# Kernel tuning notes

Hardware: AMD Instinct MI355X
Metric: run time of the kernel (lower is better)

The kernel has to match this reference:

```python
import jax, jax.numpy as jnp
import numpy as np

LAT = 512
FIN = 256
FOUT = 256
K = 3
N_STYLE = 4
B, H, W = 16, 64, 64


def setup_inputs() -> dict:
    key = jax.random.key(0)
    ks = jax.random.split(key, 8)
    x = jax.random.normal(ks[0], (B, FIN, H, W), dtype=jnp.float32)
    lat = jax.random.normal(ks[1], (B, LAT), dtype=jnp.float32)
    # main conv weight, kaiming_normal fan_in, leaky_relu a=0 -> gain sqrt(2)
    fan_in = FIN * K * K
    weight = jax.random.normal(ks[2], (FOUT, FIN, K, K), dtype=jnp.float32) * np.float32(np.sqrt(2.0 / fan_in))
    # EqualLinear layers: raw weight ~ N(0,1), runtime-scaled by 1/sqrt(in_dim)
    ws = jax.random.normal(ks[3], (N_STYLE, LAT, LAT), dtype=jnp.float32)
    bs = jnp.zeros((N_STYLE, LAT), dtype=jnp.float32)
    # final plain nn.Linear(lat_size, fin): uniform(-1/sqrt(in), 1/sqrt(in))
    bound = np.float32(1.0 / np.sqrt(LAT))
    wf = jax.random.uniform(ks[4], (FIN, LAT), dtype=jnp.float32, minval=-bound, maxval=bound)
    bf = jax.random.uniform(ks[5], (FIN,), dtype=jnp.float32, minval=-bound, maxval=bound)
    return {"x": x, "lat": lat, "weight": weight, "ws": ws, "bs": bs, "wf": wf, "bf": bf}


def reference(x, lat, weight, ws, bs, wf, bf):
    Bb, fin, Hh, Ww = x.shape
    fout, _, k, _ = weight.shape
    eq_scale = np.float32(1.0 / np.sqrt(lat.shape[1]))  # EqualLinear runtime scale

    # style MLP: n_layers_style x (EqualLinear + LeakyReLU(0.2)), then Linear -> fin
    h = lat
    for i in range(ws.shape[0]):
        h = jax.nn.leaky_relu(h @ (ws[i] * eq_scale).T + bs[i], 0.2)
    styles = h @ wf.T + bf  # [B, fin]

    # normalize base weight by inf-norm over (fin,k,k) per output channel
    wnorm = jnp.max(jnp.abs(weight), axis=(1, 2, 3), keepdims=True)
    mw = weight * (np.float32(1.0 / np.sqrt(fin * k * k)) / wnorm)  # [fout,fin,k,k]
    # normalize styles by inf-norm per sample
    styles = styles / jnp.max(jnp.abs(styles), axis=1, keepdims=True)

    # per-sample modulation + demodulation
    w = mw[None] * styles[:, None, :, None, None]  # [B,fout,fin,k,k]
    dcoefs = jax.lax.rsqrt(jnp.sum(w * w, axis=(2, 3, 4)) + 1e-8)  # [B,fout]
    w = w * dcoefs[:, :, None, None, None]
    w = w.reshape(Bb * fout, fin, k, k)

    # grouped conv with groups = batch (stride/dilation NOT passed in original -> 1)
    pad = (k - 1) // 2  # _get_same_padding with stride=1, dilation=1
    xg = x.reshape(1, Bb * fin, Hh, Ww)
    y = jax.lax.conv_general_dilated(
        xg, w, window_strides=(1, 1), padding=[(pad, pad), (pad, pad)],
        dimension_numbers=("NCHW", "OIHW", "NCHW"), feature_group_count=Bb)
    return y.reshape(Bb, fout, Hh, Ww)
```

## Files before the change

### kernel.cpp

```cpp
#include <hip/hip_runtime.h>
#include <hip/hip_bf16.h>

#define LATN 512
#define FINN 256
#define FOUTN 256
#define NB 16
#define HH 64
#define WW 64

typedef __attribute__((ext_vector_type(8))) short bf16x8;
typedef __attribute__((ext_vector_type(4))) float f32x4;
typedef __attribute__((ext_vector_type(4))) int i32x4;

#define WS_MW2    4096
#define WS_DCO    266240
#define WS_STY    282624
#define WS_WFMT   299008
#define WS_XM     1478656
#define WS_HA     (WS_XM)
#define WS_HB     (WS_XM + 32768)

__global__ void weight_prep_kernel(const float* __restrict__ weight,
                                   __hip_bfloat16* __restrict__ wfmt,
                                   float* __restrict__ mw2sum) {
    __shared__ float red[256];
    int o = blockIdx.x, t = threadIdx.x;
    const float* wrow = weight + ((size_t)o * FINN + t) * 9;
    float wv[9];
    float mx = 0.f;
    #pragma unroll
    for (int k = 0; k < 9; ++k) { wv[k] = wrow[k]; mx = fmaxf(mx, fabsf(wv[k])); }
    red[t] = mx;
    __syncthreads();
    for (int k = 128; k > 0; k >>= 1) {
        if (t < k) red[t] = fmaxf(red[t], red[t + k]);
        __syncthreads();
    }
    float scale = (1.0f / 48.0f) / red[0];
    int obi = o >> 6, ol = o & 63, ch = t >> 5, il = t & 31;
    int slot = (il >> 3) ^ ((ol >> 1) & 3);
    char* basep = (char*)wfmt + (size_t)obi * 294912 + (size_t)ch * 36864
                + (size_t)ol * 64 + slot * 16 + (il & 7) * 2;
    float s2 = 0.f;
    #pragma unroll
    for (int tap = 0; tap < 9; ++tap) {
        float m = wv[tap] * scale;
        s2 += m * m;
        *(__hip_bfloat16*)(basep + tap * 4096) = __float2bfloat16(m);
    }
    mw2sum[(size_t)o * FINN + t] = s2;
}

__global__ __launch_bounds__(256) void style_layer_kernel(
    const float* __restrict__ in, const float* __restrict__ w,
    const float* __restrict__ bias, float* __restrict__ out,
    int in_dim_v4, int out_dim, float scale, int do_lrelu) {
    int t = threadIdx.x;
    int jl = t >> 4, kl = t & 15;
    int j = blockIdx.x * 16 + jl;
    int b = blockIdx.y;
    const float4* inr = (const float4*)(in + (size_t)b * (in_dim_v4 * 4));
    const float4* wr  = (const float4*)(w + (size_t)j * (in_dim_v4 * 4));
    float sum = 0.f;
    #pragma unroll 4
    for (int kb = kl; kb < in_dim_v4; kb += 16) {
        float4 wv = wr[kb], iv = inr[kb];
        sum += wv.x * iv.x + wv.y * iv.y + wv.z * iv.z + wv.w * iv.w;
    }
    #pragma unroll
    for (int off = 8; off >= 1; off >>= 1)
        sum += __shfl_xor(sum, off, 16);
    if (kl == 0) {
        float v = sum * scale + bias[j];
        if (do_lrelu && v < 0.f) v *= 0.2f;
        out[(size_t)b * out_dim + j] = v;
    }
}

__global__ __launch_bounds__(256) void xcvt_kernel(const float* __restrict__ x,
                                                   const float* __restrict__ sty,
                                                   const float* __restrict__ mw2,
                                                   float* __restrict__ dco,
                                                   char* __restrict__ xm) {
    __shared__ float tile[64][65];
    __shared__ float styl[256];
    int h = blockIdx.x, b = blockIdx.y;
    int t = threadIdx.x;
    int lane = t & 63;
    int wl_ = t & 63, ig = t >> 6;
    const float* styb = sty + (size_t)b * FINN;
    float mxv = 0.f;
    #pragma unroll
    for (int q = 0; q < 4; ++q) mxv = fmaxf(mxv, fabsf(styb[lane + 64 * q]));
    #pragma unroll
    for (int off = 32; off >= 1; off >>= 1) mxv = fmaxf(mxv, __shfl_xor(mxv, off));
    float inv_m = 1.0f / mxv;
    styl[t] = styb[t] * inv_m;
    __syncthreads();

    if (h < 4) {
        int o_l = t >> 2, kl = t & 3;
        int o = h * 64 + o_l;
        const float4* m2r = (const float4*)(mw2 + (size_t)o * FINN) + kl * 16;
        const float4* svr = (const float4*)styl + kl * 16;
        float sum = 0.f;
        #pragma unroll
        for (int kb = 0; kb < 16; ++kb) {
            float4 a = m2r[kb], v = svr[kb];
            sum += a.x * v.x * v.x + a.y * v.y * v.y + a.z * v.z * v.z + a.w * v.w * v.w;
        }
        sum += __shfl_xor(sum, 1);
        sum += __shfl_xor(sum, 2);
        if (kl == 0) dco[(size_t)b * FOUTN + o] = rsqrtf(sum + 1e-8f);
    }

    char* xmb = xm + (size_t)b * 2097152;
    for (int icb = 0; icb < 4; ++icb) {
        if (icb) __syncthreads();
        #pragma unroll
        for (int p = 0; p < 16; ++p) {
            int i_l = p * 4 + ig;
            int i = icb * 64 + i_l;
            tile[i_l][wl_] = x[((size_t)(b * FINN + i)) * 4096 + h * 64 + wl_] * styl[i];
        }
        __syncthreads();
        #pragma unroll
        for (int rep = 0; rep < 2; ++rep) {
            int g = rep * 256 + t;
            int w = g >> 3, q8 = g & 7;
            int chunk = icb * 2 + (q8 >> 2), iq = q8 & 3;
            int slot = iq ^ (((h + 1) + ((w + 1) >> 1)) & 3);
            short tmp[8];
            #pragma unroll
            for (int j = 0; j < 8; ++j) {
                __hip_bfloat16 hb = __float2bfloat16(tile[q8 * 8 + j][w]);
                tmp[j] = *(short*)&hb;
            }
            char* dst = xmb + (size_t)chunk * 262144 + (size_t)(h * 64 + w) * 64 + slot * 16;
            *(bf16x8*)dst = *(bf16x8*)tmp;
        }
    }
}

__device__ __forceinline__ void gl_lds16(const void* g, void* l) {
    __builtin_amdgcn_global_load_lds(
        (const __attribute__((address_space(1))) unsigned int*)g,
        (__attribute__((address_space(3))) unsigned int*)l, 16, 0, 0);
}

template<int KH, int KW>
__device__ __forceinline__ void do_tap(f32x4 acc[4][8], bf16x8 rb[3][4],
                                       const char* xs, const char* wl,
                                       int wid, int l15, int lg, int wfrag) {
    constexpr int tap = KH * 3 + KW;
    bf16x8 wf[4], ra[4], nb[4];
    #pragma unroll
    for (int mt = 0; mt < 4; ++mt)
        wf[mt] = *(const bf16x8*)(wl + tap * 4096 + mt * 1024 + wfrag);
    if (KH == 0) {
        int p0 = (wid * 2) * 66 + KW + l15;
        int ba = p0 * 64 + ((lg ^ ((p0 >> 1) & 3)) << 4);
        #pragma unroll
        for (int nt = 0; nt < 4; ++nt)
            ra[nt] = *(const bf16x8*)(xs + ba + nt * 1024);
    }
    {
        int p1 = (wid * 2 + KH + 1) * 66 + KW + l15;
        int bb = p1 * 64 + ((lg ^ ((p1 >> 1) & 3)) << 4);
        #pragma unroll
        for (int nt = 0; nt < 4; ++nt)
            nb[nt] = *(const bf16x8*)(xs + bb + nt * 1024);
    }
    __builtin_amdgcn_sched_barrier(0);
    asm volatile("s_waitcnt lgkmcnt(4)" ::: "memory");
    __builtin_amdgcn_sched_barrier(0);
    __builtin_amdgcn_s_setprio(1);
    #pragma unroll
    for (int mt = 0; mt < 4; ++mt)
        #pragma unroll
        for (int nt = 0; nt < 4; ++nt)
            acc[mt][nt] = __builtin_amdgcn_mfma_f32_16x16x32_bf16(
                wf[mt], (KH == 0) ? ra[nt] : rb[KW][nt], acc[mt][nt], 0, 0, 0);
    __builtin_amdgcn_s_setprio(0);
    __builtin_amdgcn_sched_barrier(0);
    asm volatile("s_waitcnt lgkmcnt(0)" ::: "memory");
    __builtin_amdgcn_sched_barrier(0);
    __builtin_amdgcn_s_setprio(1);
    #pragma unroll
    for (int mt = 0; mt < 4; ++mt)
        #pragma unroll
        for (int nt = 0; nt < 4; ++nt)
            acc[mt][4 + nt] = __builtin_amdgcn_mfma_f32_16x16x32_bf16(
                wf[mt], nb[nt], acc[mt][4 + nt], 0, 0, 0);
    __builtin_amdgcn_s_setprio(0);
    #pragma unroll
    for (int nt = 0; nt < 4; ++nt) rb[KW][nt] = nb[nt];
}

__global__ __launch_bounds__(256, 2) void mconv_kernel(
    const char* __restrict__ xm, const char* __restrict__ wfmt,
    const float* __restrict__ dco, float* __restrict__ y) {
    __shared__ char xs[42240];
    __shared__ char wl[36864];

    int t = threadIdx.x;
    int lane = t & 63;
    int wid = t >> 6;
    int h0 = blockIdx.x * 8;
    int obi = blockIdx.y;
    int b = blockIdx.z;

    if (t < 80) {
        int r = t >> 3, sub = t & 7;
        int col = (sub >> 2) * 65, slot = sub & 3;
        *(i32x4*)(xs + ((r * 66 + col) * 4 + slot) * 16) = (i32x4){0, 0, 0, 0};
    }
    if (h0 == 0) {
        int e = t;
        *(i32x4*)(xs + ((0 * 66 + 1 + (e >> 2)) * 4 + (e & 3)) * 16) = (i32x4){0, 0, 0, 0};
    }
    if (h0 == 56) {
        int e = t;
        *(i32x4*)(xs + ((9 * 66 + 1 + (e >> 2)) * 4 + (e & 3)) * 16) = (i32x4){0, 0, 0, 0};
    }

    const char* xmb = xm + (size_t)b * 2097152 + lane * 16;
    unsigned xoff[10], xdst[10];
    #pragma unroll
    for (int q = 0; q < 10; ++q) {
        int idx = wid * 10 + q;
        int r = idx >> 2, quarter = idx & 3;
        int gh = h0 - 1 + r;
        bool v = (gh >= 0) && (gh < HH);
        xoff[q] = (unsigned)__builtin_amdgcn_readfirstlane(
            v ? (int)((gh * 64 + quarter * 16) * 64) : (int)0xFFFFFFFF);
        xdst[q] = (unsigned)__builtin_amdgcn_readfirstlane(
            (int)((r * 66 + 1) * 64 + quarter * 1024));
    }
    const char* wlane = wfmt + (size_t)obi * 294912 + lane * 16;

    f32x4 acc[4][8] = {};
    int l15 = lane & 15, lg = lane >> 4;
    int wfrag = l15 * 64 + ((lg ^ ((l15 >> 1) & 3)) << 4);

    for (int ch = 0; ch < 8; ++ch) {
        const char* xch = xmb + (size_t)ch * 262144;
        #pragma unroll
        for (int q = 0; q < 10; ++q)
            if (xoff[q] != 0xFFFFFFFFu) gl_lds16(xch + xoff[q], xs + xdst[q]);
        const char* wch = wlane + (size_t)ch * 36864;
        #pragma unroll
        for (int q = 0; q < 9; ++q)
            gl_lds16(wch + (wid + q * 4) * 1024, wl + (wid + q * 4) * 1024);
        asm volatile("s_waitcnt vmcnt(0) lgkmcnt(0)" ::: "memory");
        __builtin_amdgcn_s_barrier();
        __builtin_amdgcn_sched_barrier(0);

        {
            bf16x8 rb[3][4];
            do_tap<0, 0>(acc, rb, xs, wl, wid, l15, lg, wfrag);
            do_tap<0, 1>(acc, rb, xs, wl, wid, l15, lg, wfrag);
            do_tap<0, 2>(acc, rb, xs, wl, wid, l15, lg, wfrag);
            do_tap<1, 0>(acc, rb, xs, wl, wid, l15, lg, wfrag);
            do_tap<1, 1>(acc, rb, xs, wl, wid, l15, lg, wfrag);
            do_tap<1, 2>(acc, rb, xs, wl, wid, l15, lg, wfrag);
            do_tap<2, 0>(acc, rb, xs, wl, wid, l15, lg, wfrag);
            do_tap<2, 1>(acc, rb, xs, wl, wid, l15, lg, wfrag);
            do_tap<2, 2>(acc, rb, xs, wl, wid, l15, lg, wfrag);
        }

        __builtin_amdgcn_s_barrier();
        __builtin_amdgcn_sched_barrier(0);
    }

    const float* dcb = dco + (size_t)b * FOUTN + obi * 64;
    #pragma unroll
    for (int rr = 0; rr < 2; ++rr) {
        float* yb = y + (((size_t)b * FOUTN + obi * 64) * HH + (h0 + wid * 2 + rr)) * WW;
        #pragma unroll
        for (int mt = 0; mt < 4; ++mt) {
            #pragma unroll
            for (int j = 0; j < 4; ++j) {
                int o_l = mt * 16 + lg * 4 + j;
                float d = dcb[o_l];
                #pragma unroll
                for (int n4 = 0; n4 < 4; ++n4)
                    yb[(size_t)o_l * 4096 + n4 * 16 + l15] = acc[mt][rr * 4 + n4][j] * d;
            }
        }
    }
}

extern "C" void kernel_launch(void* const* d_in, const int* in_sizes, int n_in,
                              void* d_out, int out_size, void* d_ws, size_t ws_size,
                              hipStream_t stream) {
    const float* x      = (const float*)d_in[0];
    const float* lat    = (const float*)d_in[1];
    const float* weight = (const float*)d_in[2];
    const float* wsm    = (const float*)d_in[3];
    const float* bsm    = (const float*)d_in[4];
    const float* wff    = (const float*)d_in[5];
    const float* bff    = (const float*)d_in[6];
    float* y = (float*)d_out;

    char* base = (char*)d_ws;
    float* mw2     = (float*)(base + WS_MW2);
    float* dco     = (float*)(base + WS_DCO);
    float* sty     = (float*)(base + WS_STY);
    __hip_bfloat16* wfmt = (__hip_bfloat16*)(base + WS_WFMT);
    char* xm       = base + WS_XM;
    float* hA      = (float*)(base + WS_HA);
    float* hB      = (float*)(base + WS_HB);

    const float eq = 0.044194173824159216f;

    weight_prep_kernel<<<FOUTN, 256, 0, stream>>>(weight, wfmt, mw2);
    style_layer_kernel<<<dim3(LATN / 16, NB), 256, 0, stream>>>(
        lat, wsm + 0 * (size_t)LATN * LATN, bsm + 0 * LATN, hA, LATN / 4, LATN, eq, 1);
    style_layer_kernel<<<dim3(LATN / 16, NB), 256, 0, stream>>>(
        hA, wsm + 1 * (size_t)LATN * LATN, bsm + 1 * LATN, hB, LATN / 4, LATN, eq, 1);
    style_layer_kernel<<<dim3(LATN / 16, NB), 256, 0, stream>>>(
        hB, wsm + 2 * (size_t)LATN * LATN, bsm + 2 * LATN, hA, LATN / 4, LATN, eq, 1);
    style_layer_kernel<<<dim3(LATN / 16, NB), 256, 0, stream>>>(
        hA, wsm + 3 * (size_t)LATN * LATN, bsm + 3 * LATN, hB, LATN / 4, LATN, eq, 1);
    style_layer_kernel<<<dim3(FINN / 16, NB), 256, 0, stream>>>(
        hB, wff, bff, sty, LATN / 4, FINN, 1.0f, 0);
    xcvt_kernel<<<dim3(HH, NB), 256, 0, stream>>>(x, sty, mw2, dco, xm);
    mconv_kernel<<<dim3(8, 4, NB), 256, 0, stream>>>(xm, (const char*)wfmt, dco, y);
}
```

Before: 109.8 us.

## Fuse style scaling and bf16 conversion of x into conv kernel tile loads

New measurement: 108.7 us. About the same (-1.1%).

```diff
diff --git a/kernel.cpp b/kernel.cpp
--- a/kernel.cpp
+++ b/kernel.cpp
@@ -19,6 +19,7 @@
 #define WS_XM     1478656
 #define WS_HA     (WS_XM)
 #define WS_HB     (WS_XM + 32768)
+#define WS_SNORM  (WS_XM + 65536)
 
 __global__ void weight_prep_kernel(const float* __restrict__ weight,
                                    __hip_bfloat16* __restrict__ wfmt,
@@ -77,69 +78,32 @@
     }
 }
 
-__global__ __launch_bounds__(256) void xcvt_kernel(const float* __restrict__ x,
-                                                   const float* __restrict__ sty,
-                                                   const float* __restrict__ mw2,
-                                                   float* __restrict__ dco,
-                                                   char* __restrict__ xm) {
-    __shared__ float tile[64][65];
-    __shared__ float styl[256];
-    int h = blockIdx.x, b = blockIdx.y;
-    int t = threadIdx.x;
-    int lane = t & 63;
-    int wl_ = t & 63, ig = t >> 6;
-    const float* styb = sty + (size_t)b * FINN;
-    float mxv = 0.f;
-    #pragma unroll
-    for (int q = 0; q < 4; ++q) mxv = fmaxf(mxv, fabsf(styb[lane + 64 * q]));
-    #pragma unroll
-    for (int off = 32; off >= 1; off >>= 1) mxv = fmaxf(mxv, __shfl_xor(mxv, off));
-    float inv_m = 1.0f / mxv;
-    styl[t] = styb[t] * inv_m;
-    __syncthreads();
-
-    if (h < 4) {
-        int o_l = t >> 2, kl = t & 3;
-        int o = h * 64 + o_l;
-        const float4* m2r = (const float4*)(mw2 + (size_t)o * FINN) + kl * 16;
-        const float4* svr = (const float4*)styl + kl * 16;
-        float sum = 0.f;
-        #pragma unroll
-        for (int kb = 0; kb < 16; ++kb) {
-            float4 a = m2r[kb], v = svr[kb];
-            sum += a.x * v.x * v.x + a.y * v.y * v.y + a.z * v.z * v.z + a.w * v.w * v.w;
-        }
-        sum += __shfl_xor(sum, 1);
-        sum += __shfl_xor(sum, 2);
-        if (kl == 0) dco[(size_t)b * FOUTN + o] = rsqrtf(sum + 1e-8f);
-    }
-
-    char* xmb = xm + (size_t)b * 2097152;
-    for (int icb = 0; icb < 4; ++icb) {
-        if (icb) __syncthreads();
-        #pragma unroll
-        for (int p = 0; p < 16; ++p) {
-            int i_l = p * 4 + ig;
-            int i = icb * 64 + i_l;
-            tile[i_l][wl_] = x[((size_t)(b * FINN + i)) * 4096 + h * 64 + wl_] * styl[i];
-        }
+__global__ __launch_bounds__(256) void norm_dcoef_kernel(
+    const float* __restrict__ sty, const float* __restrict__ mw2,
+    float* __restrict__ snorm, float* __restrict__ dco) {
+    __shared__ float red[256];
+    __shared__ float s2[256];
+    int b = blockIdx.x, t = threadIdx.x;
+    float v = sty[(size_t)b * FINN + t];
+    red[t] = fabsf(v);
+    __syncthreads();
+    for (int k = 128; k > 0; k >>= 1) {
+        if (t < k) red[t] = fmaxf(red[t], red[t + k]);
         __syncthreads();
-        #pragma unroll
-        for (int rep = 0; rep < 2; ++rep) {
-            int g = rep * 256 + t;
-            int w = g >> 3, q8 = g & 7;
-            int chunk = icb * 2 + (q8 >> 2), iq = q8 & 3;
-            int slot = iq ^ (((h + 1) + ((w + 1) >> 1)) & 3);
-            short tmp[8];
-            #pragma unroll
-            for (int j = 0; j < 8; ++j) {
-                __hip_bfloat16 hb = __float2bfloat16(tile[q8 * 8 + j][w]);
-                tmp[j] = *(short*)&hb;
-            }
-            char* dst = xmb + (size_t)chunk * 262144 + (size_t)(h * 64 + w) * 64 + slot * 16;
-            *(bf16x8*)dst = *(bf16x8*)tmp;
-        }
-    }
+    }
+    float sv = v / red[0];
+    snorm[(size_t)b * FINN + t] = sv;
+    s2[t] = sv * sv;
+    __syncthreads();
+    const float4* m2 = (const float4*)(mw2 + (size_t)t * FINN);
+    const float4* sq = (const float4*)s2;
+    float sum = 0.f;
+    #pragma unroll 8
+    for (int kb = 0; kb < 64; ++kb) {
+        float4 a = m2[kb], xq = sq[kb];
+        sum += a.x * xq.x + a.y * xq.y + a.z * xq.z + a.w * xq.w;
+    }
+    dco[(size_t)b * FOUTN + t] = rsqrtf(sum + 1e-8f);
 }
 
 __device__ __forceinline__ void gl_lds16(const void* g, void* l) {
@@ -198,10 +162,12 @@
 }
 
 __global__ __launch_bounds__(256, 2) void mconv_kernel(
-    const char* __restrict__ xm, const char* __restrict__ wfmt,
-    const float* __restrict__ dco, float* __restrict__ y) {
+    const float* __restrict__ x, const char* __restrict__ wfmt,
+    const float* __restrict__ snorm, const float* __restrict__ dco,
+    float* __restrict__ y) {
     __shared__ char xs[42240];
     __shared__ char wl[36864];
+    __shared__ float styl[256];
 
     int t = threadIdx.x;
     int lane = t & 63;
@@ -215,43 +181,46 @@
         int col = (sub >> 2) * 65, slot = sub & 3;
         *(i32x4*)(xs + ((r * 66 + col) * 4 + slot) * 16) = (i32x4){0, 0, 0, 0};
     }
-    if (h0 == 0) {
-        int e = t;
-        *(i32x4*)(xs + ((0 * 66 + 1 + (e >> 2)) * 4 + (e & 3)) * 16) = (i32x4){0, 0, 0, 0};
-    }
-    if (h0 == 56) {
-        int e = t;
-        *(i32x4*)(xs + ((9 * 66 + 1 + (e >> 2)) * 4 + (e & 3)) * 16) = (i32x4){0, 0, 0, 0};
-    }
-
-    const char* xmb = xm + (size_t)b * 2097152 + lane * 16;
-    unsigned xoff[10], xdst[10];
-    #pragma unroll
-    for (int q = 0; q < 10; ++q) {
-        int idx = wid * 10 + q;
-        int r = idx >> 2, quarter = idx & 3;
-        int gh = h0 - 1 + r;
-        bool v = (gh >= 0) && (gh < HH);
-        xoff[q] = (unsigned)__builtin_amdgcn_readfirstlane(
-            v ? (int)((gh * 64 + quarter * 16) * 64) : (int)0xFFFFFFFF);
-        xdst[q] = (unsigned)__builtin_amdgcn_readfirstlane(
-            (int)((r * 66 + 1) * 64 + quarter * 1024));
-    }
+    styl[t] = snorm[(size_t)b * FINN + t];
+    __syncthreads();
+
     const char* wlane = wfmt + (size_t)obi * 294912 + lane * 16;
+    const float* xbb = x + (size_t)b * FINN * 4096;
 
     f32x4 acc[4][8] = {};
     int l15 = lane & 15, lg = lane >> 4;
     int wfrag = l15 * 64 + ((lg ^ ((l15 >> 1) & 3)) << 4);
 
     for (int ch = 0; ch < 8; ++ch) {
-        const char* xch = xmb + (size_t)ch * 262144;
-        #pragma unroll
-        for (int q = 0; q < 10; ++q)
-            if (xoff[q] != 0xFFFFFFFFu) gl_lds16(xch + xoff[q], xs + xdst[q]);
         const char* wch = wlane + (size_t)ch * 36864;
         #pragma unroll
         for (int q = 0; q < 9; ++q)
             gl_lds16(wch + (wid + q * 4) * 1024, wl + (wid + q * 4) * 1024);
+
+        {
+            float sv[8];
+            #pragma unroll
+            for (int j = 0; j < 8; ++j) sv[j] = styl[ch * 32 + wid * 8 + j];
+            const float* xq = xbb + (size_t)(ch * 32 + wid * 8) * 4096;
+            #pragma unroll
+            for (int r = 0; r < 10; ++r) {
+                int gh = h0 - 1 + r;
+                short tmp[8];
+                if (gh >= 0 && gh < HH) {
+                    #pragma unroll
+                    for (int j = 0; j < 8; ++j) {
+                        float v = xq[(size_t)j * 4096 + gh * 64 + lane] * sv[j];
+                        __hip_bfloat16 hb = __float2bfloat16(v);
+                        tmp[j] = *(short*)&hb;
+                    }
+                } else {
+                    #pragma unroll
+                    for (int j = 0; j < 8; ++j) tmp[j] = 0;
+                }
+                int s = wid ^ (((gh + 1) + ((lane + 1) >> 1)) & 3);
+                *(bf16x8*)(xs + (r * 66 + 1 + lane) * 64 + s * 16) = *(bf16x8*)tmp;
+            }
+        }
         asm volatile("s_waitcnt vmcnt(0) lgkmcnt(0)" ::: "memory");
         __builtin_amdgcn_s_barrier();
         __builtin_amdgcn_sched_barrier(0);
@@ -308,9 +277,9 @@
     float* dco     = (float*)(base + WS_DCO);
     float* sty     = (float*)(base + WS_STY);
     __hip_bfloat16* wfmt = (__hip_bfloat16*)(base + WS_WFMT);
-    char* xm       = base + WS_XM;
     float* hA      = (float*)(base + WS_HA);
     float* hB      = (float*)(base + WS_HB);
+    float* snorm   = (float*)(base + WS_SNORM);
 
     const float eq = 0.044194173824159216f;
 
@@ -325,6 +294,6 @@
         hA, wsm + 3 * (size_t)LATN * LATN, bsm + 3 * LATN, hB, LATN / 4, LATN, eq, 1);
     style_layer_kernel<<<dim3(FINN / 16, NB), 256, 0, stream>>>(
         hB, wff, bff, sty, LATN / 4, FINN, 1.0f, 0);
-    xcvt_kernel<<<dim3(HH, NB), 256, 0, stream>>>(x, sty, mw2, dco, xm);
-    mconv_kernel<<<dim3(8, 4, NB), 256, 0, stream>>>(xm, (const char*)wfmt, dco, y);
-}
+    norm_dcoef_kernel<<<NB, 256, 0, stream>>>(sty, mw2, snorm, dco);
+    mconv_kernel<<<dim3(8, 4, NB), 256, 0, stream>>>(x, (const char*)wfmt, snorm, dco, y);
+}
```
